# Kernel optimization log

Hardware: AMD Instinct MI355X
Metric: run time of the kernel (lower is better)

## Reference

```python
import jax, jax.numpy as jnp
import numpy as np

B, S, D, F, E = 4, 2048, 2048, 4096, 8


def setup_inputs() -> dict:
    key = jax.random.key(0)
    k1, k2, k3, k4 = jax.random.split(key, 4)
    hidden_states = jax.random.normal(k1, (B, S, D), dtype=jnp.float32)
    router_logits = jax.random.normal(k2, (B, S, E), dtype=jnp.float32)
    # per-expert FFN weights, scaled for stable magnitudes
    w1 = jax.random.normal(k3, (E, F, D), dtype=jnp.float32) / np.sqrt(D)
    w2 = jax.random.normal(k4, (E, D, F), dtype=jnp.float32) / np.sqrt(F)
    return {"hidden_states": hidden_states, "router_logits": router_logits, "w1": w1, "w2": w2}


def reference(hidden_states, router_logits, w1, w2):
    # Top-1 routing: each token goes to exactly one expert (argmax of logits).
    b, s, d = hidden_states.shape
    e = w1.shape[0]
    x = hidden_states.reshape(-1, d)                 # [T, D], T = B*S
    assign = jnp.argmax(router_logits.reshape(-1, e), axis=-1)  # [T] int
    out = jnp.zeros_like(x)
    # Fixed small loop over experts (structurally distinct weights);
    # each iteration: dense GEMM -> SiLU -> dense GEMM, masked combine.
    for ei in range(e):
        h = jax.nn.silu(x @ w1[ei].T) @ w2[ei].T     # [T, D]
        out = out + jnp.where((assign == ei)[:, None], h, 0.0)
    return out.reshape(b, s, d)
```

## Files before the change

### kernel.cpp

```cpp
#include <hip/hip_runtime.h>
#include <stdint.h>

#define T_TOKENS 8192
#define DDIM 2048
#define FDIM 4096
#define NEXP 8
#define MAXTILES 72

typedef __attribute__((ext_vector_type(8))) short bf16x8;
typedef __attribute__((ext_vector_type(4))) float f32x4;

__device__ __forceinline__ unsigned short f2bf(float f) {
  unsigned int u = __float_as_uint(f);
  unsigned int r = (u + 0x7FFFu + ((u >> 16) & 1u)) >> 16;
  return (unsigned short)r;
}

__global__ void k_assign(const float* __restrict__ logits,
                         int* __restrict__ assign,
                         int* __restrict__ counts) {
  int t = blockIdx.x * blockDim.x + threadIdx.x;
  if (t >= T_TOKENS) return;
  const float* l = logits + (size_t)t * NEXP;
  float bv = l[0]; int be = 0;
#pragma unroll
  for (int e = 1; e < NEXP; ++e) {
    float v = l[e];
    if (v > bv) { bv = v; be = e; }
  }
  assign[t] = be;
  atomicAdd(&counts[be], 1);
}

__global__ void k_scan(const int* __restrict__ counts,
                       int* __restrict__ offsets,
                       int* __restrict__ tile_e,
                       int* __restrict__ tile_rb,
                       int* __restrict__ ntiles) {
  if (threadIdx.x == 0) {
    int acc = 0, nt = 0;
    for (int e = 0; e < NEXP; ++e) {
      offsets[e] = acc;
      int c = counts[e];
      acc += c;
      int t = (c + 127) >> 7;
      for (int i = 0; i < t; ++i) { tile_e[nt] = e; tile_rb[nt] = i; ++nt; }
    }
    ntiles[0] = nt;
  }
}

__global__ void k_place(const int* __restrict__ assign,
                        const int* __restrict__ offsets,
                        int* __restrict__ cursors,
                        int* __restrict__ perm) {
  int t = blockIdx.x * blockDim.x + threadIdx.x;
  if (t >= T_TOKENS) return;
  int e = assign[t];
  int pos = atomicAdd(&cursors[e], 1);
  perm[offsets[e] + pos] = t;
}

__global__ void k_gather_x(const float* __restrict__ x,
                           const int* __restrict__ perm,
                           unsigned short* __restrict__ xg) {
  int idx = blockIdx.x * blockDim.x + threadIdx.x;
  int slot = idx / (DDIM / 4);
  int c4 = idx - slot * (DDIM / 4);
  int tok = perm[slot];
  float4 v = ((const float4*)(x + (size_t)tok * DDIM))[c4];
  ushort4 o;
  o.x = f2bf(v.x); o.y = f2bf(v.y); o.z = f2bf(v.z); o.w = f2bf(v.w);
  ((ushort4*)(xg + (size_t)slot * DDIM))[c4] = o;
}

__global__ void k_cast(const float* __restrict__ src,
                       unsigned short* __restrict__ dst, int n4) {
  int i = blockIdx.x * blockDim.x + threadIdx.x;
  if (i >= n4) return;
  float4 v = ((const float4*)src)[i];
  ushort4 o;
  o.x = f2bf(v.x); o.y = f2bf(v.y); o.z = f2bf(v.z); o.w = f2bf(v.w);
  ((ushort4*)dst)[i] = o;
}

__device__ __forceinline__ void glds(const unsigned short* g, unsigned short* l) {
  __builtin_amdgcn_global_load_lds(
      (const __attribute__((address_space(1))) void*)g,
      (__attribute__((address_space(3))) void*)l, 16, 0, 0);
}

template<bool FIRST>
__launch_bounds__(256)
__global__ void k_gemm(const unsigned short* __restrict__ Ap,
                       const unsigned short* __restrict__ Bw,
                       unsigned short* __restrict__ Hout,
                       float* __restrict__ Out,
                       const int* __restrict__ offsets,
                       const int* __restrict__ counts,
                       const int* __restrict__ perm,
                       const int* __restrict__ tile_e,
                       const int* __restrict__ tile_rb,
                       const int* __restrict__ ntiles) {
  constexpr int K = FIRST ? DDIM : FDIM;
  constexpr int N = FIRST ? FDIM : DDIM;
  constexpr int NSTEP = K / 32;
  const int ty = blockIdx.y;
  if (ty >= ntiles[0]) return;
  const int e  = tile_e[ty];
  const int rb = tile_rb[ty] << 7;
  const int off = offsets[e];
  const int Me = counts[e];
  const int cb = blockIdx.x << 7;

  __shared__ unsigned short At[3][128 * 32];
  __shared__ unsigned short Bt[3][128 * 32];

  const int tid = threadIdx.x;
  const int wave = tid >> 6;
  const int lane = tid & 63;
  const int wr = (wave & 1) << 6;
  const int wc = (wave >> 1) << 6;

  const int crow = lane >> 2;
  const int ckoff = (lane & 3) * 8;

  const unsigned short* gA[2];
  const unsigned short* gB[2];
#pragma unroll
  for (int c = 0; c < 2; ++c) {
    int row = wave * 32 + c * 16 + crow;
    int ar = rb + row; if (ar >= Me) ar = Me - 1;
    gA[c] = Ap + (size_t)(off + ar) * K + ckoff;
    gB[c] = Bw + (size_t)e * N * K + (size_t)(cb + row) * K + ckoff;
  }
  const int ldsoff = wave * 1024;

#pragma unroll
  for (int s = 0; s < 2; ++s) {
#pragma unroll
    for (int c = 0; c < 2; ++c) {
      glds(gA[c] + s * 32, &At[s][ldsoff + c * 512]);
      glds(gB[c] + s * 32, &Bt[s][ldsoff + c * 512]);
    }
  }

  f32x4 acc[4][4] = {};
  int s_cur = 0, s_pre = 2;
  for (int ks = 0; ks < NSTEP; ++ks) {
    asm volatile("s_waitcnt vmcnt(4) lgkmcnt(0)\n\ts_barrier" ::: "memory");

    int ka = ks + 2; if (ka >= NSTEP) ka -= NSTEP;
    const int kadd = ka * 32;
#pragma unroll
    for (int c = 0; c < 2; ++c) {
      glds(gA[c] + kadd, &At[s_pre][ldsoff + c * 512]);
      glds(gB[c] + kadd, &Bt[s_pre][ldsoff + c * 512]);
    }

    bf16x8 af[4], bfr[4];
#pragma unroll
    for (int i = 0; i < 4; ++i) {
      af[i]  = *(const bf16x8*)&At[s_cur][(wr + i * 16 + (lane & 15)) * 32 + (lane >> 4) * 8];
      bfr[i] = *(const bf16x8*)&Bt[s_cur][(wc + i * 16 + (lane & 15)) * 32 + (lane >> 4) * 8];
    }
#pragma unroll
    for (int i = 0; i < 4; ++i)
#pragma unroll
      for (int j = 0; j < 4; ++j)
        acc[i][j] = __builtin_amdgcn_mfma_f32_16x16x32_bf16(af[i], bfr[j], acc[i][j], 0, 0, 0);

    s_cur = (s_cur == 2) ? 0 : s_cur + 1;
    s_pre = (s_pre == 2) ? 0 : s_pre + 1;
  }

  const int ccol = lane & 15;
  const int cr0 = (lane >> 4) * 4;
#pragma unroll
  for (int i = 0; i < 4; ++i) {
#pragma unroll
    for (int r = 0; r < 4; ++r) {
      int row = rb + wr + i * 16 + cr0 + r;
      if (row < Me) {
        if (FIRST) {
          unsigned short* hrow = Hout + (size_t)(off + row) * N;
#pragma unroll
          for (int j = 0; j < 4; ++j) {
            float v = acc[i][j][r];
            float s = v / (1.0f + __expf(-v));
            hrow[cb + wc + j * 16 + ccol] = f2bf(s);
          }
        } else {
          int tok = perm[off + row];
          float* orow = Out + (size_t)tok * N;
#pragma unroll
          for (int j = 0; j < 4; ++j)
            orow[cb + wc + j * 16 + ccol] = acc[i][j][r];
        }
      }
    }
  }
}

extern "C" void kernel_launch(void* const* d_in, const int* in_sizes, int n_in,
                              void* d_out, int out_size, void* d_ws, size_t ws_size,
                              hipStream_t stream) {
  const float* x      = (const float*)d_in[0];
  const float* logits = (const float*)d_in[1];
  const float* w1     = (const float*)d_in[2];
  const float* w2     = (const float*)d_in[3];
  float* out = (float*)d_out;

  char* ws = (char*)d_ws;
  int* counts  = (int*)(ws + 0);
  int* offsets = (int*)(ws + 64);
  int* cursors = (int*)(ws + 128);
  int* tile_e  = (int*)(ws + 256);
  int* tile_rb = (int*)(ws + 1024);
  int* ntiles  = (int*)(ws + 2048);
  int* assign  = (int*)(ws + 4096);
  int* perm    = (int*)(ws + 4096 + T_TOKENS * 4);
  size_t p = 4096 + (size_t)2 * T_TOKENS * 4;
  p = (p + 255) & ~(size_t)255;
  unsigned short* Xg  = (unsigned short*)(ws + p); p += (size_t)T_TOKENS * DDIM * 2;
  unsigned short* W1b = (unsigned short*)(ws + p); p += (size_t)NEXP * FDIM * DDIM * 2;
  unsigned short* W2b = (unsigned short*)(ws + p); p += (size_t)NEXP * DDIM * FDIM * 2;
  unsigned short* Hb  = (unsigned short*)(ws + p); p += (size_t)T_TOKENS * FDIM * 2;
  if (ws_size < p) return;

  hipMemsetAsync(ws, 0, 4096, stream);
  k_assign<<<T_TOKENS / 256, 256, 0, stream>>>(logits, assign, counts);
  k_scan<<<1, 64, 0, stream>>>(counts, offsets, tile_e, tile_rb, ntiles);
  k_place<<<T_TOKENS / 256, 256, 0, stream>>>(assign, offsets, cursors, perm);
  k_gather_x<<<(T_TOKENS * (DDIM / 4)) / 256, 256, 0, stream>>>(x, perm, Xg);
  int n4 = NEXP * FDIM * (DDIM / 4);
  k_cast<<<n4 / 256, 256, 0, stream>>>(w1, W1b, n4);
  k_cast<<<n4 / 256, 256, 0, stream>>>(w2, W2b, n4);
  k_gemm<true><<<dim3(FDIM / 128, MAXTILES), 256, 0, stream>>>(
      Xg, W1b, Hb, nullptr, offsets, counts, perm, tile_e, tile_rb, ntiles);
  k_gemm<false><<<dim3(DDIM / 128, MAXTILES), 256, 0, stream>>>(
      Hb, W2b, nullptr, out, offsets, counts, perm, tile_e, tile_rb, ntiles);
}
```

Baseline: 1.188 ms.

## Enlarge grouped-GEMM tiles to 256-wide with 8 waves and 4-stage LDS pipeline

```diff
diff --git a/kernel.cpp b/kernel.cpp
--- a/kernel.cpp
+++ b/kernel.cpp
@@ -5,7 +5,8 @@
 #define DDIM 2048
 #define FDIM 4096
 #define NEXP 8
-#define MAXTILES 72
+#define MAXT1 40
+#define MAXT2 72
 
 typedef __attribute__((ext_vector_type(8))) short bf16x8;
 typedef __attribute__((ext_vector_type(4))) float f32x4;
@@ -34,19 +35,20 @@
 
 __global__ void k_scan(const int* __restrict__ counts,
                        int* __restrict__ offsets,
-                       int* __restrict__ tile_e,
-                       int* __restrict__ tile_rb,
-                       int* __restrict__ ntiles) {
+                       int* __restrict__ t1e, int* __restrict__ t1rb, int* __restrict__ n1,
+                       int* __restrict__ t2e, int* __restrict__ t2rb, int* __restrict__ n2) {
   if (threadIdx.x == 0) {
-    int acc = 0, nt = 0;
+    int acc = 0, a1 = 0, a2 = 0;
     for (int e = 0; e < NEXP; ++e) {
       offsets[e] = acc;
       int c = counts[e];
       acc += c;
-      int t = (c + 127) >> 7;
-      for (int i = 0; i < t; ++i) { tile_e[nt] = e; tile_rb[nt] = i; ++nt; }
+      int t1 = (c + 255) >> 8;
+      for (int i = 0; i < t1; ++i) { t1e[a1] = e; t1rb[a1] = i; ++a1; }
+      int t2 = (c + 127) >> 7;
+      for (int i = 0; i < t2; ++i) { t2e[a2] = e; t2rb[a2] = i; ++a2; }
     }
-    ntiles[0] = nt;
+    n1[0] = a1; n2[0] = a2;
   }
 }
 
@@ -91,7 +93,7 @@
 }
 
 template<bool FIRST>
-__launch_bounds__(256)
+__launch_bounds__(512, 2)
 __global__ void k_gemm(const unsigned short* __restrict__ Ap,
                        const unsigned short* __restrict__ Bw,
                        unsigned short* __restrict__ Hout,
@@ -102,100 +104,162 @@
                        const int* __restrict__ tile_e,
                        const int* __restrict__ tile_rb,
                        const int* __restrict__ ntiles) {
-  constexpr int K = FIRST ? DDIM : FDIM;
-  constexpr int N = FIRST ? FDIM : DDIM;
-  constexpr int NSTEP = K / 32;
+  constexpr int K   = FIRST ? DDIM : FDIM;
+  constexpr int N   = FIRST ? FDIM : DDIM;
+  constexpr int MW  = FIRST ? 8 : 4;
+  constexpr int BM  = MW * 32;
+  constexpr int NS  = K / 32;
+  constexpr int RA  = MW / 4;
+  constexpr int ASL = BM * 32;
+  constexpr int BSL = 256 * 32;
+
   const int ty = blockIdx.y;
   if (ty >= ntiles[0]) return;
-  const int e  = tile_e[ty];
-  const int rb = tile_rb[ty] << 7;
+  const int e   = tile_e[ty];
+  const int rb  = tile_rb[ty] * BM;
   const int off = offsets[e];
-  const int Me = counts[e];
-  const int cb = blockIdx.x << 7;
-
-  __shared__ unsigned short At[3][128 * 32];
-  __shared__ unsigned short Bt[3][128 * 32];
-
-  const int tid = threadIdx.x;
+  const int Me  = counts[e];
+  const int cb  = blockIdx.x << 8;
+
+  extern __shared__ unsigned short sm[];
+  unsigned short* At = sm;
+  unsigned short* Bt = sm + 4 * ASL;
+
+  const int tid  = threadIdx.x;
   const int wave = tid >> 6;
   const int lane = tid & 63;
-  const int wr = (wave & 1) << 6;
-  const int wc = (wave >> 1) << 6;
-
-  const int crow = lane >> 2;
-  const int ckoff = (lane & 3) * 8;
-
-  const unsigned short* gA[2];
+  const int wr   = wave >> 2;
+  const int wc   = wave & 3;
+
+  const int tq  = tid >> 2;
+  const int kd8 = (((tid & 3) ^ ((tid >> 3) & 3)) << 3);
+
+  const unsigned short* gA[RA];
+#pragma unroll
+  for (int r = 0; r < RA; ++r) {
+    int ar = rb + r * 128 + tq;
+    if (ar >= Me) ar = Me - 1;
+    gA[r] = Ap + (size_t)(off + ar) * K + kd8;
+  }
   const unsigned short* gB[2];
 #pragma unroll
-  for (int c = 0; c < 2; ++c) {
-    int row = wave * 32 + c * 16 + crow;
-    int ar = rb + row; if (ar >= Me) ar = Me - 1;
-    gA[c] = Ap + (size_t)(off + ar) * K + ckoff;
-    gB[c] = Bw + (size_t)e * N * K + (size_t)(cb + row) * K + ckoff;
-  }
-  const int ldsoff = wave * 1024;
-
-#pragma unroll
-  for (int s = 0; s < 2; ++s) {
-#pragma unroll
-    for (int c = 0; c < 2; ++c) {
-      glds(gA[c] + s * 32, &At[s][ldsoff + c * 512]);
-      glds(gB[c] + s * 32, &Bt[s][ldsoff + c * 512]);
+  for (int r = 0; r < 2; ++r)
+    gB[r] = Bw + (size_t)e * N * K + (size_t)(cb + r * 128 + tq) * K + kd8;
+
+  const int dlo = (wave * 16) * 32;
+  const int dhi = dlo + 128 * 32;
+
+#pragma unroll
+  for (int s = 0; s < 3; ++s) {
+#pragma unroll
+    for (int r = 0; r < RA; ++r)
+      glds(gA[r] + s * 32, At + s * ASL + dlo + r * (128 * 32));
+#pragma unroll
+    for (int r = 0; r < 2; ++r)
+      glds(gB[r] + s * 32, Bt + s * BSL + dlo + r * (128 * 32));
+  }
+  if constexpr (MW == 8) { asm volatile("s_waitcnt vmcnt(8)" ::: "memory"); }
+  else                   { asm volatile("s_waitcnt vmcnt(6)" ::: "memory"); }
+  __builtin_amdgcn_s_barrier();
+  asm volatile("" ::: "memory");
+
+  const int kswz8 = (((lane >> 4) ^ ((lane >> 1) & 3)) << 3);
+  const int aoff  = (wr * (BM / 2) + (lane & 15)) * 32 + kswz8;
+  const int boff  = (wc * 64 + (lane & 15)) * 32 + kswz8;
+
+  f32x4 acc[MW][4] = {};
+
+  for (int ks = 0; ks < NS; ++ks) {
+    const int cur = ks & 3;
+    const int pre = (ks + 3) & 3;
+    int ka = ks + 3; if (ka >= NS) ka -= NS;
+    const int ko = ka * 32;
+    const unsigned short* Ac = At + cur * ASL + aoff;
+    const unsigned short* Bc = Bt + cur * BSL + boff;
+    unsigned short* Aw = At + pre * ASL;
+    unsigned short* Bp = Bt + pre * BSL;
+
+    bf16x8 af[MW], bf[4];
+    if constexpr (MW == 8) {
+#pragma unroll
+      for (int n = 0; n < 4; ++n) bf[n] = *(const bf16x8*)(Bc + n * 512);
+#pragma unroll
+      for (int m = 0; m < 4; ++m) af[m] = *(const bf16x8*)(Ac + m * 512);
+      glds(gA[0] + ko, Aw + dlo);
+      glds(gA[1] + ko, Aw + dhi);
+      __builtin_amdgcn_s_barrier();
+      asm volatile("s_waitcnt lgkmcnt(0)" ::: "memory");
+      __builtin_amdgcn_sched_barrier(0);
+      __builtin_amdgcn_s_setprio(1);
+#pragma unroll
+      for (int m = 0; m < 4; ++m)
+#pragma unroll
+        for (int n = 0; n < 4; ++n)
+          acc[m][n] = __builtin_amdgcn_mfma_f32_16x16x32_bf16(af[m], bf[n], acc[m][n], 0, 0, 0);
+      __builtin_amdgcn_s_setprio(0);
+      __builtin_amdgcn_s_barrier();
+#pragma unroll
+      for (int m = 4; m < 8; ++m) af[m] = *(const bf16x8*)(Ac + m * 512);
+      glds(gB[0] + ko, Bp + dlo);
+      glds(gB[1] + ko, Bp + dhi);
+      asm volatile("s_waitcnt vmcnt(8)" ::: "memory");
+      __builtin_amdgcn_s_barrier();
+      asm volatile("s_waitcnt lgkmcnt(0)" ::: "memory");
+      __builtin_amdgcn_sched_barrier(0);
+      __builtin_amdgcn_s_setprio(1);
+#pragma unroll
+      for (int m = 4; m < 8; ++m)
+#pragma unroll
+        for (int n = 0; n < 4; ++n)
+          acc[m][n] = __builtin_amdgcn_mfma_f32_16x16x32_bf16(af[m], bf[n], acc[m][n], 0, 0, 0);
+      __builtin_amdgcn_s_setprio(0);
+      __builtin_amdgcn_s_barrier();
+    } else {
+#pragma unroll
+      for (int n = 0; n < 4; ++n) bf[n] = *(const bf16x8*)(Bc + n * 512);
+#pragma unroll
+      for (int m = 0; m < 4; ++m) af[m] = *(const bf16x8*)(Ac + m * 512);
+      glds(gA[0] + ko, Aw + dlo);
+      glds(gB[0] + ko, Bp + dlo);
+      glds(gB[1] + ko, Bp + dhi);
+      asm volatile("s_waitcnt vmcnt(6)" ::: "memory");
+      __builtin_amdgcn_s_barrier();
+      asm volatile("s_waitcnt lgkmcnt(0)" ::: "memory");
+      __builtin_amdgcn_sched_barrier(0);
+      __builtin_amdgcn_s_setprio(1);
+#pragma unroll
+      for (int m = 0; m < 4; ++m)
+#pragma unroll
+        for (int n = 0; n < 4; ++n)
+          acc[m][n] = __builtin_amdgcn_mfma_f32_16x16x32_bf16(af[m], bf[n], acc[m][n], 0, 0, 0);
+      __builtin_amdgcn_s_setprio(0);
+      __builtin_amdgcn_s_barrier();
     }
-  }
-
-  f32x4 acc[4][4] = {};
-  int s_cur = 0, s_pre = 2;
-  for (int ks = 0; ks < NSTEP; ++ks) {
-    asm volatile("s_waitcnt vmcnt(4) lgkmcnt(0)\n\ts_barrier" ::: "memory");
-
-    int ka = ks + 2; if (ka >= NSTEP) ka -= NSTEP;
-    const int kadd = ka * 32;
-#pragma unroll
-    for (int c = 0; c < 2; ++c) {
-      glds(gA[c] + kadd, &At[s_pre][ldsoff + c * 512]);
-      glds(gB[c] + kadd, &Bt[s_pre][ldsoff + c * 512]);
-    }
-
-    bf16x8 af[4], bfr[4];
-#pragma unroll
-    for (int i = 0; i < 4; ++i) {
-      af[i]  = *(const bf16x8*)&At[s_cur][(wr + i * 16 + (lane & 15)) * 32 + (lane >> 4) * 8];
-      bfr[i] = *(const bf16x8*)&Bt[s_cur][(wc + i * 16 + (lane & 15)) * 32 + (lane >> 4) * 8];
-    }
-#pragma unroll
-    for (int i = 0; i < 4; ++i)
-#pragma unroll
-      for (int j = 0; j < 4; ++j)
-        acc[i][j] = __builtin_amdgcn_mfma_f32_16x16x32_bf16(af[i], bfr[j], acc[i][j], 0, 0, 0);
-
-    s_cur = (s_cur == 2) ? 0 : s_cur + 1;
-    s_pre = (s_pre == 2) ? 0 : s_pre + 1;
   }
 
   const int ccol = lane & 15;
   const int cr0 = (lane >> 4) * 4;
-#pragma unroll
-  for (int i = 0; i < 4; ++i) {
+  const int colbase = cb + wc * 64;
+#pragma unroll
+  for (int i = 0; i < MW; ++i) {
 #pragma unroll
     for (int r = 0; r < 4; ++r) {
-      int row = rb + wr + i * 16 + cr0 + r;
+      int row = rb + wr * (BM / 2) + i * 16 + cr0 + r;
       if (row < Me) {
-        if (FIRST) {
+        if constexpr (FIRST) {
           unsigned short* hrow = Hout + (size_t)(off + row) * N;
 #pragma unroll
           for (int j = 0; j < 4; ++j) {
             float v = acc[i][j][r];
             float s = v / (1.0f + __expf(-v));
-            hrow[cb + wc + j * 16 + ccol] = f2bf(s);
+            hrow[colbase + j * 16 + ccol] = f2bf(s);
           }
         } else {
           int tok = perm[off + row];
           float* orow = Out + (size_t)tok * N;
 #pragma unroll
           for (int j = 0; j < 4; ++j)
-            orow[cb + wc + j * 16 + ccol] = acc[i][j][r];
+            orow[colbase + j * 16 + ccol] = acc[i][j][r];
         }
       }
     }
@@ -215,9 +279,12 @@
   int* counts  = (int*)(ws + 0);
   int* offsets = (int*)(ws + 64);
   int* cursors = (int*)(ws + 128);
-  int* tile_e  = (int*)(ws + 256);
-  int* tile_rb = (int*)(ws + 1024);
-  int* ntiles  = (int*)(ws + 2048);
+  int* t1e  = (int*)(ws + 256);
+  int* t1rb = (int*)(ws + 512);
+  int* n1   = (int*)(ws + 768);
+  int* t2e  = (int*)(ws + 1024);
+  int* t2rb = (int*)(ws + 1536);
+  int* n2   = (int*)(ws + 1856);
   int* assign  = (int*)(ws + 4096);
   int* perm    = (int*)(ws + 4096 + T_TOKENS * 4);
   size_t p = 4096 + (size_t)2 * T_TOKENS * 4;
@@ -228,16 +295,21 @@
   unsigned short* Hb  = (unsigned short*)(ws + p); p += (size_t)T_TOKENS * FDIM * 2;
   if (ws_size < p) return;
 
+  hipFuncSetAttribute(reinterpret_cast<const void*>(k_gemm<true>),
+                      hipFuncAttributeMaxDynamicSharedMemorySize, 131072);
+  hipFuncSetAttribute(reinterpret_cast<const void*>(k_gemm<false>),
+                      hipFuncAttributeMaxDynamicSharedMemorySize, 131072);
+
   hipMemsetAsync(ws, 0, 4096, stream);
   k_assign<<<T_TOKENS / 256, 256, 0, stream>>>(logits, assign, counts);
-  k_scan<<<1, 64, 0, stream>>>(counts, offsets, tile_e, tile_rb, ntiles);
+  k_scan<<<1, 64, 0, stream>>>(counts, offsets, t1e, t1rb, n1, t2e, t2rb, n2);
   k_place<<<T_TOKENS / 256, 256, 0, stream>>>(assign, offsets, cursors, perm);
   k_gather_x<<<(T_TOKENS * (DDIM / 4)) / 256, 256, 0, stream>>>(x, perm, Xg);
   int n4 = NEXP * FDIM * (DDIM / 4);
   k_cast<<<n4 / 256, 256, 0, stream>>>(w1, W1b, n4);
   k_cast<<<n4 / 256, 256, 0, stream>>>(w2, W2b, n4);
-  k_gemm<true><<<dim3(FDIM / 128, MAXTILES), 256, 0, stream>>>(
-      Xg, W1b, Hb, nullptr, offsets, counts, perm, tile_e, tile_rb, ntiles);
-  k_gemm<false><<<dim3(DDIM / 128, MAXTILES), 256, 0, stream>>>(
-      Hb, W2b, nullptr, out, offsets, counts, perm, tile_e, tile_rb, ntiles);
-}
+  k_gemm<true><<<dim3(FDIM / 256, MAXT1), 512, 131072, stream>>>(
+      Xg, W1b, Hb, nullptr, offsets, counts, perm, t1e, t1rb, n1);
+  k_gemm<false><<<dim3(DDIM / 256, MAXT2), 512, 98304, stream>>>(
+      Hb, W2b, nullptr, out, offsets, counts, perm, t2e, t2rb, n2);
+}
```

Result: faster. 1.067 ms (-10.1%).

## Enlarge GEMM tile to 128x256 with 8 waves, swizzled LDS, and fused weight cast

Applied to the files above, without the earlier changes.

```diff
diff --git a/kernel.cpp b/kernel.cpp
--- a/kernel.cpp
+++ b/kernel.cpp
@@ -64,24 +64,32 @@
 __global__ void k_gather_x(const float* __restrict__ x,
                            const int* __restrict__ perm,
                            unsigned short* __restrict__ xg) {
-  int idx = blockIdx.x * blockDim.x + threadIdx.x;
-  int slot = idx / (DDIM / 4);
-  int c4 = idx - slot * (DDIM / 4);
-  int tok = perm[slot];
-  float4 v = ((const float4*)(x + (size_t)tok * DDIM))[c4];
-  ushort4 o;
-  o.x = f2bf(v.x); o.y = f2bf(v.y); o.z = f2bf(v.z); o.w = f2bf(v.w);
-  ((ushort4*)(xg + (size_t)slot * DDIM))[c4] = o;
-}
-
-__global__ void k_cast(const float* __restrict__ src,
-                       unsigned short* __restrict__ dst, int n4) {
-  int i = blockIdx.x * blockDim.x + threadIdx.x;
-  if (i >= n4) return;
-  float4 v = ((const float4*)src)[i];
-  ushort4 o;
-  o.x = f2bf(v.x); o.y = f2bf(v.y); o.z = f2bf(v.z); o.w = f2bf(v.w);
-  ((ushort4*)dst)[i] = o;
+  const int total = T_TOKENS * (DDIM / 4);
+  const int stride = gridDim.x * blockDim.x;
+  for (int idx = blockIdx.x * blockDim.x + threadIdx.x; idx < total; idx += stride) {
+    int slot = idx / (DDIM / 4);
+    int c4 = idx - slot * (DDIM / 4);
+    int tok = perm[slot];
+    float4 v = ((const float4*)(x + (size_t)tok * DDIM))[c4];
+    ushort4 o;
+    o.x = f2bf(v.x); o.y = f2bf(v.y); o.z = f2bf(v.z); o.w = f2bf(v.w);
+    ((ushort4*)(xg + (size_t)slot * DDIM))[c4] = o;
+  }
+}
+
+__global__ void k_cast2(const float* __restrict__ s1, const float* __restrict__ s2,
+                        unsigned short* __restrict__ d1, unsigned short* __restrict__ d2,
+                        int n4) {
+  const int stride = gridDim.x * blockDim.x;
+  for (int i = blockIdx.x * blockDim.x + threadIdx.x; i < 2 * n4; i += stride) {
+    float4 v;
+    if (i < n4) v = ((const float4*)s1)[i];
+    else        v = ((const float4*)s2)[i - n4];
+    ushort4 o;
+    o.x = f2bf(v.x); o.y = f2bf(v.y); o.z = f2bf(v.z); o.w = f2bf(v.w);
+    if (i < n4) ((ushort4*)d1)[i] = o;
+    else        ((ushort4*)d2)[i - n4] = o;
+  }
 }
 
 __device__ __forceinline__ void glds(const unsigned short* g, unsigned short* l) {
@@ -91,7 +99,7 @@
 }
 
 template<bool FIRST>
-__launch_bounds__(256)
+__launch_bounds__(512, 4)
 __global__ void k_gemm(const unsigned short* __restrict__ Ap,
                        const unsigned short* __restrict__ Bw,
                        unsigned short* __restrict__ Hout,
@@ -102,100 +110,112 @@
                        const int* __restrict__ tile_e,
                        const int* __restrict__ tile_rb,
                        const int* __restrict__ ntiles) {
-  constexpr int K = FIRST ? DDIM : FDIM;
-  constexpr int N = FIRST ? FDIM : DDIM;
-  constexpr int NSTEP = K / 32;
+  constexpr int K   = FIRST ? DDIM : FDIM;
+  constexpr int N   = FIRST ? FDIM : DDIM;
+  constexpr int NS  = K / 32;
+  constexpr int ASL = 128 * 32;
+  constexpr int BSL = 256 * 32;
+
   const int ty = blockIdx.y;
   if (ty >= ntiles[0]) return;
-  const int e  = tile_e[ty];
-  const int rb = tile_rb[ty] << 7;
+  const int e   = tile_e[ty];
+  const int rb  = tile_rb[ty] << 7;
   const int off = offsets[e];
-  const int Me = counts[e];
-  const int cb = blockIdx.x << 7;
-
-  __shared__ unsigned short At[3][128 * 32];
-  __shared__ unsigned short Bt[3][128 * 32];
-
-  const int tid = threadIdx.x;
+  const int Me  = counts[e];
+  const int cb  = blockIdx.x << 8;
+
+  extern __shared__ unsigned short sm[];
+  unsigned short* At = sm;
+  unsigned short* Bt = sm + 3 * ASL;
+
+  const int tid  = threadIdx.x;
   const int wave = tid >> 6;
   const int lane = tid & 63;
-  const int wr = (wave & 1) << 6;
-  const int wc = (wave >> 1) << 6;
-
-  const int crow = lane >> 2;
-  const int ckoff = (lane & 3) * 8;
-
-  const unsigned short* gA[2];
-  const unsigned short* gB[2];
-#pragma unroll
-  for (int c = 0; c < 2; ++c) {
-    int row = wave * 32 + c * 16 + crow;
-    int ar = rb + row; if (ar >= Me) ar = Me - 1;
-    gA[c] = Ap + (size_t)(off + ar) * K + ckoff;
-    gB[c] = Bw + (size_t)e * N * K + (size_t)(cb + row) * K + ckoff;
-  }
-  const int ldsoff = wave * 1024;
+  const int wr   = wave >> 2;
+  const int wc   = wave & 3;
+
+  const int tq  = tid >> 2;
+  const int kd8 = (((tid & 3) ^ ((tid >> 3) & 3)) << 3);
+
+  int ar = rb + tq; if (ar >= Me) ar = Me - 1;
+  const unsigned short* gA  = Ap + (size_t)(off + ar) * K + kd8;
+  const unsigned short* gB0 = Bw + (size_t)e * N * K + (size_t)(cb + tq) * K + kd8;
+  const unsigned short* gB1 = gB0 + (size_t)128 * K;
+
+  const int dlo = wave * 512;
 
 #pragma unroll
   for (int s = 0; s < 2; ++s) {
-#pragma unroll
-    for (int c = 0; c < 2; ++c) {
-      glds(gA[c] + s * 32, &At[s][ldsoff + c * 512]);
-      glds(gB[c] + s * 32, &Bt[s][ldsoff + c * 512]);
-    }
-  }
+    glds(gA  + s * 32, At + s * ASL + dlo);
+    glds(gB0 + s * 32, Bt + s * BSL + dlo);
+    glds(gB1 + s * 32, Bt + s * BSL + dlo + 128 * 32);
+  }
+  asm volatile("s_waitcnt vmcnt(3)" ::: "memory");
+  __builtin_amdgcn_s_barrier();
+  asm volatile("" ::: "memory");
+
+  const int kswz8 = (((lane >> 4) ^ ((lane >> 1) & 3)) << 3);
+  const int aoff  = (wr * 64 + (lane & 15)) * 32 + kswz8;
+  const int boff  = (wc * 64 + (lane & 15)) * 32 + kswz8;
 
   f32x4 acc[4][4] = {};
-  int s_cur = 0, s_pre = 2;
-  for (int ks = 0; ks < NSTEP; ++ks) {
-    asm volatile("s_waitcnt vmcnt(4) lgkmcnt(0)\n\ts_barrier" ::: "memory");
-
-    int ka = ks + 2; if (ka >= NSTEP) ka -= NSTEP;
-    const int kadd = ka * 32;
-#pragma unroll
-    for (int c = 0; c < 2; ++c) {
-      glds(gA[c] + kadd, &At[s_pre][ldsoff + c * 512]);
-      glds(gB[c] + kadd, &Bt[s_pre][ldsoff + c * 512]);
-    }
-
-    bf16x8 af[4], bfr[4];
-#pragma unroll
-    for (int i = 0; i < 4; ++i) {
-      af[i]  = *(const bf16x8*)&At[s_cur][(wr + i * 16 + (lane & 15)) * 32 + (lane >> 4) * 8];
-      bfr[i] = *(const bf16x8*)&Bt[s_cur][(wc + i * 16 + (lane & 15)) * 32 + (lane >> 4) * 8];
-    }
-#pragma unroll
-    for (int i = 0; i < 4; ++i)
-#pragma unroll
-      for (int j = 0; j < 4; ++j)
-        acc[i][j] = __builtin_amdgcn_mfma_f32_16x16x32_bf16(af[i], bfr[j], acc[i][j], 0, 0, 0);
-
-    s_cur = (s_cur == 2) ? 0 : s_cur + 1;
-    s_pre = (s_pre == 2) ? 0 : s_pre + 1;
+  int cur = 0, pre = 2;
+  for (int ks = 0; ks < NS; ++ks) {
+    int ka = ks + 2; if (ka >= NS) ka -= NS;
+    const int ko = ka * 32;
+    const unsigned short* Ac = At + cur * ASL + aoff;
+    const unsigned short* Bc = Bt + cur * BSL + boff;
+
+    bf16x8 af[4], bf[4];
+#pragma unroll
+    for (int m = 0; m < 4; ++m) af[m] = *(const bf16x8*)(Ac + m * 512);
+#pragma unroll
+    for (int n = 0; n < 4; ++n) bf[n] = *(const bf16x8*)(Bc + n * 512);
+
+    glds(gA  + ko, At + pre * ASL + dlo);
+    glds(gB0 + ko, Bt + pre * BSL + dlo);
+    glds(gB1 + ko, Bt + pre * BSL + dlo + 128 * 32);
+
+    asm volatile("s_waitcnt vmcnt(3)" ::: "memory");
+    __builtin_amdgcn_s_barrier();
+    asm volatile("s_waitcnt lgkmcnt(0)" ::: "memory");
+    __builtin_amdgcn_sched_barrier(0);
+    __builtin_amdgcn_s_setprio(1);
+#pragma unroll
+    for (int m = 0; m < 4; ++m)
+#pragma unroll
+      for (int n = 0; n < 4; ++n)
+        acc[m][n] = __builtin_amdgcn_mfma_f32_16x16x32_bf16(af[m], bf[n], acc[m][n], 0, 0, 0);
+    __builtin_amdgcn_s_setprio(0);
+    __builtin_amdgcn_s_barrier();
+
+    cur = (cur == 2) ? 0 : cur + 1;
+    pre = (pre == 2) ? 0 : pre + 1;
   }
 
   const int ccol = lane & 15;
   const int cr0 = (lane >> 4) * 4;
+  const int colbase = cb + wc * 64;
 #pragma unroll
   for (int i = 0; i < 4; ++i) {
 #pragma unroll
     for (int r = 0; r < 4; ++r) {
-      int row = rb + wr + i * 16 + cr0 + r;
+      int row = rb + wr * 64 + i * 16 + cr0 + r;
       if (row < Me) {
-        if (FIRST) {
+        if constexpr (FIRST) {
           unsigned short* hrow = Hout + (size_t)(off + row) * N;
 #pragma unroll
           for (int j = 0; j < 4; ++j) {
             float v = acc[i][j][r];
             float s = v / (1.0f + __expf(-v));
-            hrow[cb + wc + j * 16 + ccol] = f2bf(s);
+            hrow[colbase + j * 16 + ccol] = f2bf(s);
           }
         } else {
           int tok = perm[off + row];
           float* orow = Out + (size_t)tok * N;
 #pragma unroll
           for (int j = 0; j < 4; ++j)
-            orow[cb + wc + j * 16 + ccol] = acc[i][j][r];
+            orow[colbase + j * 16 + ccol] = acc[i][j][r];
         }
       }
     }
@@ -228,16 +248,20 @@
   unsigned short* Hb  = (unsigned short*)(ws + p); p += (size_t)T_TOKENS * FDIM * 2;
   if (ws_size < p) return;
 
+  hipFuncSetAttribute(reinterpret_cast<const void*>(k_gemm<true>),
+                      hipFuncAttributeMaxDynamicSharedMemorySize, 73728);
+  hipFuncSetAttribute(reinterpret_cast<const void*>(k_gemm<false>),
+                      hipFuncAttributeMaxDynamicSharedMemorySize, 73728);
+
   hipMemsetAsync(ws, 0, 4096, stream);
   k_assign<<<T_TOKENS / 256, 256, 0, stream>>>(logits, assign, counts);
   k_scan<<<1, 64, 0, stream>>>(counts, offsets, tile_e, tile_rb, ntiles);
   k_place<<<T_TOKENS / 256, 256, 0, stream>>>(assign, offsets, cursors, perm);
-  k_gather_x<<<(T_TOKENS * (DDIM / 4)) / 256, 256, 0, stream>>>(x, perm, Xg);
+  k_gather_x<<<2048, 256, 0, stream>>>(x, perm, Xg);
   int n4 = NEXP * FDIM * (DDIM / 4);
-  k_cast<<<n4 / 256, 256, 0, stream>>>(w1, W1b, n4);
-  k_cast<<<n4 / 256, 256, 0, stream>>>(w2, W2b, n4);
-  k_gemm<true><<<dim3(FDIM / 128, MAXTILES), 256, 0, stream>>>(
+  k_cast2<<<2048, 256, 0, stream>>>(w1, w2, W1b, W2b, n4);
+  k_gemm<true><<<dim3(FDIM / 256, MAXTILES), 512, 73728, stream>>>(
       Xg, W1b, Hb, nullptr, offsets, counts, perm, tile_e, tile_rb, ntiles);
-  k_gemm<false><<<dim3(DDIM / 128, MAXTILES), 256, 0, stream>>>(
+  k_gemm<false><<<dim3(DDIM / 256, MAXTILES), 512, 73728, stream>>>(
       Hb, W2b, nullptr, out, offsets, counts, perm, tile_e, tile_rb, ntiles);
 }
```

After: 1.068 ms. 1.11x faster.
